# Optimization experiments

Measured on AMD Instinct MI355X. Metric: run time of the kernel, lower is better.

## Reference

```python
import jax, jax.numpy as jnp
import numpy as np

NUM_NODES = 100000
NUM_REL = 500
D = 400          # entity_out_dim[0] * nheads_GAT[0] = 200 * 2
C = 50           # conv_out_channels
B = 16384        # batch of triples


def setup_inputs() -> dict:
    key = jax.random.key(0)
    k = jax.random.split(key, 7)
    entity_emb = jax.random.normal(k[0], (NUM_NODES, D), jnp.float32)
    relation_emb = jax.random.normal(k[1], (NUM_REL, D), jnp.float32)
    # Conv2d(1, C, (1, 3)) weight: [C, 1, 1, 3]; xavier-ish scale
    conv_w = jax.random.normal(k[2], (C, 1, 1, 3), jnp.float32) * 0.5
    conv_b = jnp.zeros((C,), jnp.float32)
    # Linear(D*C, 1)
    fc_w = jax.random.normal(k[3], (1, D * C), jnp.float32) * 0.01
    fc_b = jnp.zeros((1,), jnp.float32)
    heads = jax.random.randint(k[4], (B,), 0, NUM_NODES)
    rels = jax.random.randint(k[5], (B,), 0, NUM_REL)
    tails = jax.random.randint(k[6], (B,), 0, NUM_NODES)
    batch_inputs = jnp.stack([heads, rels, tails], axis=1)  # [B, 3]
    return {
        "entity_emb": entity_emb,
        "relation_emb": relation_emb,
        "conv_w": conv_w,
        "conv_b": conv_b,
        "fc_w": fc_w,
        "fc_b": fc_b,
        "batch_inputs": batch_inputs,
    }


def reference(entity_emb, relation_emb, conv_w, conv_b, fc_w, fc_b, batch_inputs):
    # Gather (h, r, t) rows: irregular access into large tables
    h = entity_emb[batch_inputs[:, 0]]    # [B, D]
    r = relation_emb[batch_inputs[:, 1]]  # [B, D]
    t = entity_emb[batch_inputs[:, 2]]    # [B, D]
    # torch: cat -> [B, 3, D], transpose -> [B, D, 3], unsqueeze -> [B, 1, D, 3]
    x = jnp.stack([h, r, t], axis=-1)     # [B, D, 3]
    # Conv2d(1, C, (1, 3)): kernel spans full width -> per-channel dot over 3
    w = conv_w[:, 0, 0, :]                # [C, 3]
    out = jnp.einsum("bdk,ck->bcd", x, w) + conv_b[None, :, None]  # [B, C, D]
    out = jax.nn.relu(out)                # dropout is identity in eval mode
    # squeeze(-1).view(B, -1): channel-major flatten -> [B, C*D]
    flat = out.reshape(out.shape[0], -1)
    return flat @ fc_w.T + fc_b           # [B, 1]
```

## Files before the change

### kernel.cpp

```cpp
#include <hip/hip_runtime.h>


typedef _Float16 h2 __attribute__((ext_vector_type(2)));

constexpr int D    = 400;
constexpr int C    = 50;
constexpr int CP   = C / 2;
constexpr int DPAD = D + 4;

static __device__ __forceinline__ float dot2acc(h2 a, h2 b, float c) {
#if __has_builtin(__builtin_amdgcn_fdot2)
    return __builtin_amdgcn_fdot2(a, b, c, false);
#else
    h2 p = a * b;
    return c + (float)p[0] + (float)p[1];
#endif
}

__global__ __attribute__((amdgpu_flat_work_group_size(512, 512), amdgpu_waves_per_eu(2, 4)))
void grcnet_pk16c(
    const float* __restrict__ entity_emb,
    const float* __restrict__ relation_emb,
    const float* __restrict__ conv_w,
    const float* __restrict__ conv_b,
    const float* __restrict__ fc_w,
    const float* __restrict__ fc_b,
    const int*   __restrict__ batch_inputs,
    float* __restrict__ out,
    int nB)
{
    __shared__ h2    fc_lds[CP][DPAD];
    __shared__ h2    conv_lds[CP][4];
    __shared__ float partials[2][4][4];

    const int tid  = threadIdx.x;
    const int lane = tid & 63;
    const int wv   = tid >> 6;
    const int grp  = wv >> 1;
    const int hc   = wv & 1;
    const int b0   = blockIdx.x * 16;
    if (b0 >= nB) return;

    for (int k = tid; k < CP * D; k += 512) {
        const int cp = k / D;
        const int d  = k - cp * D;
        h2 g;
        g[0] = (_Float16)fc_w[(2*cp)     * D + d];
        g[1] = (_Float16)fc_w[(2*cp + 1) * D + d];
        fc_lds[cp][d] = g;
    }
    if (tid < CP * 4) {
        h2 z; z[0] = (_Float16)0; z[1] = (_Float16)0;
        fc_lds[tid >> 2][D + (tid & 3)] = z;
    }
    if (tid < CP) {
        const int c0 = 2 * tid;
        h2 wa; wa[0] = (_Float16)conv_w[3*c0+0]; wa[1] = (_Float16)conv_w[3*c0+3];
        h2 wb; wb[0] = (_Float16)conv_w[3*c0+1]; wb[1] = (_Float16)conv_w[3*c0+4];
        h2 wc; wc[0] = (_Float16)conv_w[3*c0+2]; wc[1] = (_Float16)conv_w[3*c0+5];
        h2 cb; cb[0] = (_Float16)conv_b[c0];     cb[1] = (_Float16)conv_b[c0+1];
        conv_lds[tid][0] = wa; conv_lds[tid][1] = wb;
        conv_lds[tid][2] = wc; conv_lds[tid][3] = cb;
    }
    __syncthreads();

    const int bbase = __builtin_amdgcn_readfirstlane(b0 + 4 * grp);
    const int* bi = batch_inputs + 3 * bbase;
    const float* eh0 = entity_emb   + (size_t)bi[0]  * D;
    const float* er0 = relation_emb + (size_t)bi[1]  * D;
    const float* et0 = entity_emb   + (size_t)bi[2]  * D;
    const float* eh1 = entity_emb   + (size_t)bi[3]  * D;
    const float* er1 = relation_emb + (size_t)bi[4]  * D;
    const float* et1 = entity_emb   + (size_t)bi[5]  * D;
    const float* eh2 = entity_emb   + (size_t)bi[6]  * D;
    const float* er2 = relation_emb + (size_t)bi[7]  * D;
    const float* et2 = entity_emb   + (size_t)bi[8]  * D;
    const float* eh3 = entity_emb   + (size_t)bi[9]  * D;
    const float* er3 = relation_emb + (size_t)bi[10] * D;
    const float* et3 = entity_emb   + (size_t)bi[11] * D;

    float acc0 = 0.f, acc1 = 0.f, acc2 = 0.f, acc3 = 0.f;
    const h2 zero2 = (h2)(_Float16)0;

    #define BODY(C0, C1)                                                          \
    {                                                                             \
        constexpr int NC = (C1) - (C0);                                           \
        h2 cwa[NC], cwb[NC], cwcv[NC], ccb[NC];                                   \
        _Pragma("unroll")                                                         \
        for (int j = 0; j < NC; ++j) {                                            \
            cwa[j]  = conv_lds[(C0) + j][0];                                      \
            cwb[j]  = conv_lds[(C0) + j][1];                                      \
            cwcv[j] = conv_lds[(C0) + j][2];                                      \
            ccb[j]  = conv_lds[(C0) + j][3];                                      \
        }                                                                         \
        _Pragma("unroll 1")                                                       \
        for (int i = 0; i < 7; ++i) {                                             \
            const int d  = lane + 64 * i;                                         \
            const bool a = (d < D);                                               \
            const int dc = a ? d : 0;                   \
            const int dp = a ? d : D;                   \
            const char* fcol = (const char*)&fc_lds[C0][dp];                      \
            _Float16 v;                                                           \
            h2 h0, r0, t0, h1, r1, t1, h2_, r2, t2, h3, r3, t3;                   \
            v = (_Float16)eh0[dc]; h0[0]=v;  h0[1]=v;                             \
            v = (_Float16)er0[dc]; r0[0]=v;  r0[1]=v;                             \
            v = (_Float16)et0[dc]; t0[0]=v;  t0[1]=v;                             \
            v = (_Float16)eh1[dc]; h1[0]=v;  h1[1]=v;                             \
            v = (_Float16)er1[dc]; r1[0]=v;  r1[1]=v;                             \
            v = (_Float16)et1[dc]; t1[0]=v;  t1[1]=v;                             \
            v = (_Float16)eh2[dc]; h2_[0]=v; h2_[1]=v;                            \
            v = (_Float16)er2[dc]; r2[0]=v;  r2[1]=v;                             \
            v = (_Float16)et2[dc]; t2[0]=v;  t2[1]=v;                             \
            v = (_Float16)eh3[dc]; h3[0]=v;  h3[1]=v;                             \
            v = (_Float16)er3[dc]; r3[0]=v;  r3[1]=v;                             \
            v = (_Float16)et3[dc]; t3[0]=v;  t3[1]=v;                             \
            _Pragma("unroll")                                                     \
            for (int j = 0; j < NC; ++j) {                                        \
                const h2 f2 = *(const h2*)(fcol + (size_t)(j * (DPAD * 4)));      \
                h2 s0 = h0 *cwa[j] + (r0*cwb[j] + (t0*cwcv[j] + ccb[j]));         \
                h2 s1 = h1 *cwa[j] + (r1*cwb[j] + (t1*cwcv[j] + ccb[j]));         \
                h2 s2 = h2_*cwa[j] + (r2*cwb[j] + (t2*cwcv[j] + ccb[j]));         \
                h2 s3 = h3 *cwa[j] + (r3*cwb[j] + (t3*cwcv[j] + ccb[j]));         \
                s0 = __builtin_elementwise_max(s0, zero2);                        \
                s1 = __builtin_elementwise_max(s1, zero2);                        \
                s2 = __builtin_elementwise_max(s2, zero2);                        \
                s3 = __builtin_elementwise_max(s3, zero2);                        \
                acc0 = dot2acc(s0, f2, acc0);                                     \
                acc1 = dot2acc(s1, f2, acc1);                                     \
                acc2 = dot2acc(s2, f2, acc2);                                     \
                acc3 = dot2acc(s3, f2, acc3);                                     \
            }                                                                     \
        }                                                                         \
    }

    if (hc == 0) { BODY(0, 13) } else { BODY(13, 25) }
    #undef BODY

    #pragma unroll
    for (int off = 32; off > 0; off >>= 1) {
        acc0 += __shfl_xor(acc0, off);
        acc1 += __shfl_xor(acc1, off);
        acc2 += __shfl_xor(acc2, off);
        acc3 += __shfl_xor(acc3, off);
    }
    if (lane == 0) {
        partials[hc][grp][0] = acc0; partials[hc][grp][1] = acc1;
        partials[hc][grp][2] = acc2; partials[hc][grp][3] = acc3;
    }
    __syncthreads();

    if (tid < 16) {
        const int g = tid >> 2, j = tid & 3;
        out[b0 + 4*g + j] = partials[0][g][j] + partials[1][g][j] + fc_b[0];
    }
}

extern "C" void kernel_launch(void* const* d_in, const int* in_sizes, int n_in,
                              void* d_out, int out_size, void* d_ws, size_t ws_size,
                              hipStream_t stream) {
    const float* entity_emb   = (const float*)d_in[0];
    const float* relation_emb = (const float*)d_in[1];
    const float* conv_w       = (const float*)d_in[2];
    const float* conv_b       = (const float*)d_in[3];
    const float* fc_w         = (const float*)d_in[4];
    const float* fc_b         = (const float*)d_in[5];
    const int*   batch_inputs = (const int*)d_in[6];
    float* out = (float*)d_out;

    const int nB = in_sizes[6] / 3;
    const int blocks = (nB + 15) / 16;
    grcnet_pk16c<<<blocks, 512, 0, stream>>>(
        entity_emb, relation_emb, conv_w, conv_b, fc_w, fc_b, batch_inputs, out, nB);
}
```

Measured before the change: 49.48 us.

## Software-pipeline embedding gathers with double-buffered registers and vectorize fc_w staging

The d-loop is fully unrolled into seven chunks. Gather loads for the next chunk are issued into a second register set while the current chunk computes, which is meant to hide global-memory latency on the irregular row gathers. The fc_w staging into LDS now uses float4 loads and 16-byte LDS stores instead of scalar ones. The tail chunk uses a precomputed index that points past-the-end lanes at zeroed padding. Register pressure goes up, which could lower occupancy.

```diff
diff --git a/kernel.cpp b/kernel.cpp
--- a/kernel.cpp
+++ b/kernel.cpp
@@ -2,23 +2,25 @@
 
 
 typedef _Float16 h2 __attribute__((ext_vector_type(2)));
+typedef _Float16 h8 __attribute__((ext_vector_type(8)));
 
 constexpr int D    = 400;
-constexpr int C    = 50;
-constexpr int CP   = C / 2;
-constexpr int DPAD = D + 4;
+constexpr int CP   = 25;
+constexpr int DPAD = 404;
 
 static __device__ __forceinline__ float dot2acc(h2 a, h2 b, float c) {
 #if __has_builtin(__builtin_amdgcn_fdot2)
     return __builtin_amdgcn_fdot2(a, b, c, false);
 #else
-    h2 p = a * b;
-    return c + (float)p[0] + (float)p[1];
+    h2 p = a * b; return c + (float)p[0] + (float)p[1];
 #endif
+}
+static __device__ __forceinline__ h2 dup(float v) {
+    _Float16 x = (_Float16)v; h2 r; r[0] = x; r[1] = x; return r;
 }
 
 __global__ __attribute__((amdgpu_flat_work_group_size(512, 512), amdgpu_waves_per_eu(2, 4)))
-void grcnet_pk16c(
+void grcnet_pk16d(
     const float* __restrict__ entity_emb,
     const float* __restrict__ relation_emb,
     const float* __restrict__ conv_w,
@@ -41,13 +43,17 @@
     const int b0   = blockIdx.x * 16;
     if (b0 >= nB) return;
 
-    for (int k = tid; k < CP * D; k += 512) {
-        const int cp = k / D;
-        const int d  = k - cp * D;
-        h2 g;
-        g[0] = (_Float16)fc_w[(2*cp)     * D + d];
-        g[1] = (_Float16)fc_w[(2*cp + 1) * D + d];
-        fc_lds[cp][d] = g;
+    for (int k = tid; k < CP * 100; k += 512) {
+        const int cp = k / 100;
+        const int dq = k - cp * 100;
+        const float4 A  = *(const float4*)(fc_w + (2*cp)     * D + 4*dq);
+        const float4 Bv = *(const float4*)(fc_w + (2*cp + 1) * D + 4*dq);
+        h8 g;
+        g[0]=(_Float16)A.x; g[1]=(_Float16)Bv.x;
+        g[2]=(_Float16)A.y; g[3]=(_Float16)Bv.y;
+        g[4]=(_Float16)A.z; g[5]=(_Float16)Bv.z;
+        g[6]=(_Float16)A.w; g[7]=(_Float16)Bv.w;
+        *(h8*)&fc_lds[cp][4*dq] = g;
     }
     if (tid < CP * 4) {
         h2 z; z[0] = (_Float16)0; z[1] = (_Float16)0;
@@ -55,86 +61,97 @@
     }
     if (tid < CP) {
         const int c0 = 2 * tid;
-        h2 wa; wa[0] = (_Float16)conv_w[3*c0+0]; wa[1] = (_Float16)conv_w[3*c0+3];
-        h2 wb; wb[0] = (_Float16)conv_w[3*c0+1]; wb[1] = (_Float16)conv_w[3*c0+4];
-        h2 wc; wc[0] = (_Float16)conv_w[3*c0+2]; wc[1] = (_Float16)conv_w[3*c0+5];
-        h2 cb; cb[0] = (_Float16)conv_b[c0];     cb[1] = (_Float16)conv_b[c0+1];
-        conv_lds[tid][0] = wa; conv_lds[tid][1] = wb;
-        conv_lds[tid][2] = wc; conv_lds[tid][3] = cb;
+        h2 wa, wb, wc, cb;
+        wa[0]=(_Float16)conv_w[3*c0+0]; wa[1]=(_Float16)conv_w[3*c0+3];
+        wb[0]=(_Float16)conv_w[3*c0+1]; wb[1]=(_Float16)conv_w[3*c0+4];
+        wc[0]=(_Float16)conv_w[3*c0+2]; wc[1]=(_Float16)conv_w[3*c0+5];
+        cb[0]=(_Float16)conv_b[c0];     cb[1]=(_Float16)conv_b[c0+1];
+        conv_lds[tid][0]=wa; conv_lds[tid][1]=wb;
+        conv_lds[tid][2]=wc; conv_lds[tid][3]=cb;
     }
     __syncthreads();
 
     const int bbase = __builtin_amdgcn_readfirstlane(b0 + 4 * grp);
     const int* bi = batch_inputs + 3 * bbase;
-    const float* eh0 = entity_emb   + (size_t)bi[0]  * D;
-    const float* er0 = relation_emb + (size_t)bi[1]  * D;
-    const float* et0 = entity_emb   + (size_t)bi[2]  * D;
-    const float* eh1 = entity_emb   + (size_t)bi[3]  * D;
-    const float* er1 = relation_emb + (size_t)bi[4]  * D;
-    const float* et1 = entity_emb   + (size_t)bi[5]  * D;
-    const float* eh2 = entity_emb   + (size_t)bi[6]  * D;
-    const float* er2 = relation_emb + (size_t)bi[7]  * D;
-    const float* et2 = entity_emb   + (size_t)bi[8]  * D;
-    const float* eh3 = entity_emb   + (size_t)bi[9]  * D;
-    const float* er3 = relation_emb + (size_t)bi[10] * D;
-    const float* et3 = entity_emb   + (size_t)bi[11] * D;
+    const float* p0h = entity_emb   + (size_t)bi[0]  * D + lane;
+    const float* p0r = relation_emb + (size_t)bi[1]  * D + lane;
+    const float* p0t = entity_emb   + (size_t)bi[2]  * D + lane;
+    const float* p1h = entity_emb   + (size_t)bi[3]  * D + lane;
+    const float* p1r = relation_emb + (size_t)bi[4]  * D + lane;
+    const float* p1t = entity_emb   + (size_t)bi[5]  * D + lane;
+    const float* p2h = entity_emb   + (size_t)bi[6]  * D + lane;
+    const float* p2r = relation_emb + (size_t)bi[7]  * D + lane;
+    const float* p2t = entity_emb   + (size_t)bi[8]  * D + lane;
+    const float* p3h = entity_emb   + (size_t)bi[9]  * D + lane;
+    const float* p3r = relation_emb + (size_t)bi[10] * D + lane;
+    const float* p3t = entity_emb   + (size_t)bi[11] * D + lane;
+
+    const int  d6  = lane + 384;
+    const bool a6  = (d6 < D);
+    const int  i6  = a6 ? 384 : -lane;
+    const h2*  fcb  = (const h2*)fc_lds + lane;
+    const h2*  fcb6 = (const h2*)fc_lds + (a6 ? d6 : D);
 
     float acc0 = 0.f, acc1 = 0.f, acc2 = 0.f, acc3 = 0.f;
     const h2 zero2 = (h2)(_Float16)0;
 
-    #define BODY(C0, C1)                                                          \
+    #define LOADI(S, IDX)                                                         \
+        f##S##_0h = p0h[IDX]; f##S##_0r = p0r[IDX]; f##S##_0t = p0t[IDX];         \
+        f##S##_1h = p1h[IDX]; f##S##_1r = p1r[IDX]; f##S##_1t = p1t[IDX];         \
+        f##S##_2h = p2h[IDX]; f##S##_2r = p2r[IDX]; f##S##_2t = p2t[IDX];         \
+        f##S##_3h = p3h[IDX]; f##S##_3r = p3r[IDX]; f##S##_3t = p3t[IDX];
+
+    #define COMPUTE(S, FB, FIDX0)                                                 \
     {                                                                             \
-        constexpr int NC = (C1) - (C0);                                           \
-        h2 cwa[NC], cwb[NC], cwcv[NC], ccb[NC];                                   \
+        const h2 H0 = dup(f##S##_0h), R0 = dup(f##S##_0r), T0 = dup(f##S##_0t);   \
+        const h2 H1 = dup(f##S##_1h), R1 = dup(f##S##_1r), T1 = dup(f##S##_1t);   \
+        const h2 H2 = dup(f##S##_2h), R2 = dup(f##S##_2r), T2 = dup(f##S##_2t);   \
+        const h2 H3 = dup(f##S##_3h), R3 = dup(f##S##_3r), T3 = dup(f##S##_3t);   \
         _Pragma("unroll")                                                         \
         for (int j = 0; j < NC; ++j) {                                            \
-            cwa[j]  = conv_lds[(C0) + j][0];                                      \
-            cwb[j]  = conv_lds[(C0) + j][1];                                      \
-            cwcv[j] = conv_lds[(C0) + j][2];                                      \
-            ccb[j]  = conv_lds[(C0) + j][3];                                      \
-        }                                                                         \
-        _Pragma("unroll 1")                                                       \
-        for (int i = 0; i < 7; ++i) {                                             \
-            const int d  = lane + 64 * i;                                         \
-            const bool a = (d < D);                                               \
-            const int dc = a ? d : 0;                   \
-            const int dp = a ? d : D;                   \
-            const char* fcol = (const char*)&fc_lds[C0][dp];                      \
-            _Float16 v;                                                           \
-            h2 h0, r0, t0, h1, r1, t1, h2_, r2, t2, h3, r3, t3;                   \
-            v = (_Float16)eh0[dc]; h0[0]=v;  h0[1]=v;                             \
-            v = (_Float16)er0[dc]; r0[0]=v;  r0[1]=v;                             \
-            v = (_Float16)et0[dc]; t0[0]=v;  t0[1]=v;                             \
-            v = (_Float16)eh1[dc]; h1[0]=v;  h1[1]=v;                             \
-            v = (_Float16)er1[dc]; r1[0]=v;  r1[1]=v;                             \
-            v = (_Float16)et1[dc]; t1[0]=v;  t1[1]=v;                             \
-            v = (_Float16)eh2[dc]; h2_[0]=v; h2_[1]=v;                            \
-            v = (_Float16)er2[dc]; r2[0]=v;  r2[1]=v;                             \
-            v = (_Float16)et2[dc]; t2[0]=v;  t2[1]=v;                             \
-            v = (_Float16)eh3[dc]; h3[0]=v;  h3[1]=v;                             \
-            v = (_Float16)er3[dc]; r3[0]=v;  r3[1]=v;                             \
-            v = (_Float16)et3[dc]; t3[0]=v;  t3[1]=v;                             \
-            _Pragma("unroll")                                                     \
-            for (int j = 0; j < NC; ++j) {                                        \
-                const h2 f2 = *(const h2*)(fcol + (size_t)(j * (DPAD * 4)));      \
-                h2 s0 = h0 *cwa[j] + (r0*cwb[j] + (t0*cwcv[j] + ccb[j]));         \
-                h2 s1 = h1 *cwa[j] + (r1*cwb[j] + (t1*cwcv[j] + ccb[j]));         \
-                h2 s2 = h2_*cwa[j] + (r2*cwb[j] + (t2*cwcv[j] + ccb[j]));         \
-                h2 s3 = h3 *cwa[j] + (r3*cwb[j] + (t3*cwcv[j] + ccb[j]));         \
-                s0 = __builtin_elementwise_max(s0, zero2);                        \
-                s1 = __builtin_elementwise_max(s1, zero2);                        \
-                s2 = __builtin_elementwise_max(s2, zero2);                        \
-                s3 = __builtin_elementwise_max(s3, zero2);                        \
-                acc0 = dot2acc(s0, f2, acc0);                                     \
-                acc1 = dot2acc(s1, f2, acc1);                                     \
-                acc2 = dot2acc(s2, f2, acc2);                                     \
-                acc3 = dot2acc(s3, f2, acc3);                                     \
-            }                                                                     \
+            const h2 f2 = (FB)[(FIDX0) + (C0 + j) * DPAD];        \
+            h2 s0 = H0*cwa[j] + (R0*cwb[j] + (T0*cwc[j] + ccb[j]));               \
+            h2 s1 = H1*cwa[j] + (R1*cwb[j] + (T1*cwc[j] + ccb[j]));               \
+            h2 s2 = H2*cwa[j] + (R2*cwb[j] + (T2*cwc[j] + ccb[j]));               \
+            h2 s3 = H3*cwa[j] + (R3*cwb[j] + (T3*cwc[j] + ccb[j]));               \
+            s0 = __builtin_elementwise_max(s0, zero2);                            \
+            s1 = __builtin_elementwise_max(s1, zero2);                            \
+            s2 = __builtin_elementwise_max(s2, zero2);                            \
+            s3 = __builtin_elementwise_max(s3, zero2);                            \
+            acc0 = dot2acc(s0, f2, acc0);                                         \
+            acc1 = dot2acc(s1, f2, acc1);                                         \
+            acc2 = dot2acc(s2, f2, acc2);                                         \
+            acc3 = dot2acc(s3, f2, acc3);                                         \
         }                                                                         \
     }
 
-    if (hc == 0) { BODY(0, 13) } else { BODY(13, 25) }
+    #define BODY(C0_, NC_)                                                        \
+    {                                                                             \
+        constexpr int C0 = (C0_), NC = (NC_);                                     \
+        h2 cwa[NC], cwb[NC], cwc[NC], ccb[NC];                                    \
+        _Pragma("unroll")                                                         \
+        for (int j = 0; j < NC; ++j) {                                            \
+            cwa[j] = conv_lds[C0+j][0]; cwb[j] = conv_lds[C0+j][1];               \
+            cwc[j] = conv_lds[C0+j][2]; ccb[j] = conv_lds[C0+j][3];               \
+        }                                                                         \
+        float fA_0h, fA_0r, fA_0t, fA_1h, fA_1r, fA_1t;                           \
+        float fA_2h, fA_2r, fA_2t, fA_3h, fA_3r, fA_3t;                           \
+        float fB_0h, fB_0r, fB_0t, fB_1h, fB_1r, fB_1t;                           \
+        float fB_2h, fB_2r, fB_2t, fB_3h, fB_3r, fB_3t;                           \
+        LOADI(A, 0)                                                               \
+        LOADI(B, 64)   COMPUTE(A, fcb, 0*64)                                      \
+        LOADI(A, 128)  COMPUTE(B, fcb, 1*64)                                      \
+        LOADI(B, 192)  COMPUTE(A, fcb, 2*64)                                      \
+        LOADI(A, 256)  COMPUTE(B, fcb, 3*64)                                      \
+        LOADI(B, 320)  COMPUTE(A, fcb, 4*64)                                      \
+        LOADI(A, i6)   COMPUTE(B, fcb, 5*64)                                      \
+                       COMPUTE(A, fcb6, 0)                                        \
+    }
+
+    if (hc == 0) { BODY(0, 13) } else { BODY(13, 12) }
     #undef BODY
+    #undef COMPUTE
+    #undef LOADI
 
     #pragma unroll
     for (int off = 32; off > 0; off >>= 1) {
@@ -169,6 +186,6 @@
 
     const int nB = in_sizes[6] / 3;
     const int blocks = (nB + 15) / 16;
-    grcnet_pk16c<<<blocks, 512, 0, stream>>>(
+    grcnet_pk16d<<<blocks, 512, 0, stream>>>(
         entity_emb, relation_emb, conv_w, conv_b, fc_w, fc_b, batch_inputs, out, nB);
 }
```

Result: faster. 45.73 us (-7.6%).
